# Optimization experiments

Hardware: AMD Instinct MI355X
Metric: run time of the kernel (lower is better)

The kernel has to match this reference:

```python
import jax, jax.numpy as jnp
import numpy as np

NUM_EMB = 10_000_000
EMB_DIM = 3
B = 16384
HIST = 50
K = 128


def setup_inputs() -> dict:
    key = jax.random.key(0)
    k1, k2, k3, k4, k5, k6, k7, k8, k9 = jax.random.split(key, 9)
    eb_input = jax.random.randint(k1, (B * HIST,), 0, NUM_EMB, dtype=jnp.int64)
    eb_offset = (jnp.arange(B, dtype=jnp.int64) * HIST)  # bag starts
    mlp_input = jax.random.normal(k2, (B, K), dtype=jnp.float32)
    # learned params
    emb_weight = jax.random.normal(k3, (NUM_EMB, EMB_DIM), dtype=jnp.float32)
    w0 = jax.random.normal(k4, (12, K), dtype=jnp.float32) * (1.0 / np.sqrt(K))
    b0 = jax.random.normal(k5, (12,), dtype=jnp.float32) * 0.01
    w1 = jax.random.normal(k6, (6, 12), dtype=jnp.float32) * (1.0 / np.sqrt(12))
    b1 = jax.random.normal(k7, (6,), dtype=jnp.float32) * 0.01
    w2 = jax.random.normal(k8, (3, 6), dtype=jnp.float32) * (1.0 / np.sqrt(6))
    b2 = jax.random.normal(k9, (3,), dtype=jnp.float32) * 0.01
    return {"eb_input": eb_input, "eb_offset": eb_offset, "mlp_input": mlp_input,
            "emb_weight": emb_weight, "w0": w0, "b0": b0, "w1": w1, "b1": b1,
            "w2": w2, "b2": b2}


def _embedding_bag_mean(weight, indices, offsets, num_bags):
    # bag id for each index position (offsets are sorted bag starts, offsets[0]=0)
    n = indices.shape[0]
    seg = jnp.searchsorted(offsets, jnp.arange(n, dtype=offsets.dtype), side='right') - 1
    rows = weight[indices]                                   # [N, 3] gather
    sums = jax.ops.segment_sum(rows, seg, num_segments=num_bags)          # [B, 3]
    cnts = jax.ops.segment_sum(jnp.ones((n,), weight.dtype), seg, num_segments=num_bags)
    return sums / jnp.maximum(cnts, 1.0)[:, None]            # mean mode; empty bag -> 0


def reference(eb_input, eb_offset, mlp_input, emb_weight, w0, b0, w1, b1, w2, b2):
    # All 3 EmbeddingBags alias the SAME module (python list * 3), so one lookup suffices.
    eb_out = _embedding_bag_mean(emb_weight, eb_input, eb_offset, mlp_input.shape[0])
    h = mlp_input @ w0.T + b0
    h = h @ w1.T + b1
    mlp_out = h @ w2.T + b2                                   # [B, 3]
    return jnp.concatenate([eb_out, eb_out, eb_out, mlp_out], axis=1)  # [B, 12]
```

## Files before the change

kernel.cpp:

```cpp
#include <hip/hip_runtime.h>


#define KDIM 128

__global__ __launch_bounds__(KDIM) void collapse_weights_kernel(
    const float* __restrict__ w0, const float* __restrict__ b0,
    const float* __restrict__ w1, const float* __restrict__ b1,
    const float* __restrict__ w2, const float* __restrict__ b2,
    float* __restrict__ ws)
{
    __shared__ float t[6][KDIM];
    __shared__ float tb[6];

    const int k = threadIdx.x;
    for (int i = 0; i < 6; ++i) {
        float acc = 0.f;
        for (int j = 0; j < 12; ++j)
            acc += w1[i * 12 + j] * w0[j * KDIM + k];
        t[i][k] = acc;
    }
    if (k < 6) {
        float acc = 0.f;
        for (int j = 0; j < 12; ++j)
            acc += w1[k * 12 + j] * b0[j];
        tb[k] = acc + b1[k];
    }
    __syncthreads();

    for (int o = 0; o < 3; ++o) {
        float acc = 0.f;
        for (int i = 0; i < 6; ++i)
            acc += w2[o * 6 + i] * t[i][k];
        ws[o * KDIM + k] = acc;
    }
    if (k == 0) {
        for (int o = 0; o < 3; ++o) {
            float acc = 0.f;
            for (int i = 0; i < 6; ++i)
                acc += w2[o * 6 + i] * tb[i];
            ws[3 * KDIM + o] = acc + b2[o];
        }
    }
}

__global__ __launch_bounds__(256) void fused_embbag_mlp_kernel(
    const int* __restrict__ eb_input,
    const int* __restrict__ eb_offset,
    const float* __restrict__ mlp_input,
    const float* __restrict__ emb_weight,
    const float* __restrict__ ws,
    float* __restrict__ out,
    int n_indices, int num_bags)
{
    const int lane = threadIdx.x & 63;
    const int wave = threadIdx.x >> 6;
    const int bag  = blockIdx.x * (blockDim.x >> 6) + wave;
    if (bag >= num_bags) return;

    const int start = eb_offset[bag];
    const int end   = (bag + 1 < num_bags) ? eb_offset[bag + 1] : n_indices;

    float s0 = 0.f, s1 = 0.f, s2 = 0.f;
    for (int i = start + lane; i < end; i += 64) {
        const int idx = eb_input[i];
        const float* r = emb_weight + (long long)idx * 3;
        s0 += r[0];
        s1 += r[1];
        s2 += r[2];
    }

    const float* x = mlp_input + (long long)bag * KDIM;
    const float2 xv = *(const float2*)(x + 2 * lane);
    const int c = 2 * lane;
    float m0 = xv.x * ws[0 * KDIM + c] + xv.y * ws[0 * KDIM + c + 1];
    float m1 = xv.x * ws[1 * KDIM + c] + xv.y * ws[1 * KDIM + c + 1];
    float m2 = xv.x * ws[2 * KDIM + c] + xv.y * ws[2 * KDIM + c + 1];

    #pragma unroll
    for (int off = 32; off > 0; off >>= 1) {
        s0 += __shfl_xor(s0, off, 64);
        s1 += __shfl_xor(s1, off, 64);
        s2 += __shfl_xor(s2, off, 64);
        m0 += __shfl_xor(m0, off, 64);
        m1 += __shfl_xor(m1, off, 64);
        m2 += __shfl_xor(m2, off, 64);
    }

    const float cnt = (float)(end - start);
    const float inv = 1.0f / fmaxf(cnt, 1.0f);
    const float e0 = s0 * inv, e1 = s1 * inv, e2 = s2 * inv;
    const float o9  = m0 + ws[3 * KDIM + 0];
    const float o10 = m1 + ws[3 * KDIM + 1];
    const float o11 = m2 + ws[3 * KDIM + 2];

    if (lane < 12) {
        float v;
        if (lane < 9) {
            const int r3 = lane - (lane >= 3 ? (lane >= 6 ? 6 : 3) : 0);
            v = (r3 == 0) ? e0 : (r3 == 1 ? e1 : e2);
        } else {
            v = (lane == 9) ? o9 : (lane == 10 ? o10 : o11);
        }
        out[(long long)bag * 12 + lane] = v;
    }
}

extern "C" void kernel_launch(void* const* d_in, const int* in_sizes, int n_in,
                              void* d_out, int out_size, void* d_ws, size_t ws_size,
                              hipStream_t stream) {
    const int*   eb_input   = (const int*)d_in[0];
    const int*   eb_offset  = (const int*)d_in[1];
    const float* mlp_input  = (const float*)d_in[2];
    const float* emb_weight = (const float*)d_in[3];
    const float* w0 = (const float*)d_in[4];
    const float* b0 = (const float*)d_in[5];
    const float* w1 = (const float*)d_in[6];
    const float* b1 = (const float*)d_in[7];
    const float* w2 = (const float*)d_in[8];
    const float* b2 = (const float*)d_in[9];
    float* out = (float*)d_out;
    float* ws  = (float*)d_ws;

    const int n_indices = in_sizes[0];
    const int num_bags  = in_sizes[1];

    collapse_weights_kernel<<<1, KDIM, 0, stream>>>(w0, b0, w1, b1, w2, b2, ws);

    const int waves_per_block = 4;
    const int grid = (num_bags + waves_per_block - 1) / waves_per_block;
    fused_embbag_mlp_kernel<<<grid, 256, 0, stream>>>(
        eb_input, eb_offset, mlp_input, emb_weight, ws, out, n_indices, num_bags);
}
```

Measured before the change: 198.5 us.

## Remap lanes to per-column gather and halve shuffle reduction work

Each wave now assigns lanes by (row group, embedding column), so each lane gathers a single float per row across 16 row groups instead of three floats per row. The MLP dot product is likewise split so each lane computes 8 elements for one output column with float4 loads. The cross-lane reduction then only reduces two values over 4 shuffle steps instead of six values over 6 steps, and the output write uses a direct lane-to-column mapping. In exchange each lane runs more loop iterations over the bag, which can expose more serialized gather latency, and one lane in four sits idle.

Result: no change. 199.7 us (+0.6%).

```diff
diff --git a/kernel.cpp b/kernel.cpp
--- a/kernel.cpp
+++ b/kernel.cpp
@@ -57,51 +57,40 @@
     const int bag  = blockIdx.x * (blockDim.x >> 6) + wave;
     if (bag >= num_bags) return;
 
+    const int c = lane & 3;
+    const int q = lane >> 2;
+
     const int start = eb_offset[bag];
     const int end   = (bag + 1 < num_bags) ? eb_offset[bag + 1] : n_indices;
+    const int cnt   = end - start;
 
-    float s0 = 0.f, s1 = 0.f, s2 = 0.f;
-    for (int i = start + lane; i < end; i += 64) {
-        const int idx = eb_input[i];
-        const float* r = emb_weight + (long long)idx * 3;
-        s0 += r[0];
-        s1 += r[1];
-        s2 += r[2];
+    float s = 0.f;
+    float m = 0.f;
+
+    if (c < 3) {
+        for (int row = q; row < cnt; row += 16) {
+            const int idx = eb_input[start + row];
+            s += emb_weight[(long long)idx * 3 + c];
+        }
+        const float4* xp = (const float4*)(mlp_input + (long long)bag * KDIM + q * 8);
+        const float4* wp = (const float4*)(ws + c * KDIM + q * 8);
+        const float4 x0 = xp[0], x1 = xp[1];
+        const float4 wv0 = wp[0], wv1 = wp[1];
+        m = x0.x * wv0.x + x0.y * wv0.y + x0.z * wv0.z + x0.w * wv0.w
+          + x1.x * wv1.x + x1.y * wv1.y + x1.z * wv1.z + x1.w * wv1.w;
     }
 
-    const float* x = mlp_input + (long long)bag * KDIM;
-    const float2 xv = *(const float2*)(x + 2 * lane);
-    const int c = 2 * lane;
-    float m0 = xv.x * ws[0 * KDIM + c] + xv.y * ws[0 * KDIM + c + 1];
-    float m1 = xv.x * ws[1 * KDIM + c] + xv.y * ws[1 * KDIM + c + 1];
-    float m2 = xv.x * ws[2 * KDIM + c] + xv.y * ws[2 * KDIM + c + 1];
-
     #pragma unroll
-    for (int off = 32; off > 0; off >>= 1) {
-        s0 += __shfl_xor(s0, off, 64);
-        s1 += __shfl_xor(s1, off, 64);
-        s2 += __shfl_xor(s2, off, 64);
-        m0 += __shfl_xor(m0, off, 64);
-        m1 += __shfl_xor(m1, off, 64);
-        m2 += __shfl_xor(m2, off, 64);
+    for (int off = 4; off <= 32; off <<= 1) {
+        s += __shfl_xor(s, off, 64);
+        m += __shfl_xor(m, off, 64);
     }
 
-    const float cnt = (float)(end - start);
-    const float inv = 1.0f / fmaxf(cnt, 1.0f);
-    const float e0 = s0 * inv, e1 = s1 * inv, e2 = s2 * inv;
-    const float o9  = m0 + ws[3 * KDIM + 0];
-    const float o10 = m1 + ws[3 * KDIM + 1];
-    const float o11 = m2 + ws[3 * KDIM + 2];
-
-    if (lane < 12) {
-        float v;
-        if (lane < 9) {
-            const int r3 = lane - (lane >= 3 ? (lane >= 6 ? 6 : 3) : 0);
-            v = (r3 == 0) ? e0 : (r3 == 1 ? e1 : e2);
-        } else {
-            v = (lane == 9) ? o9 : (lane == 10 ? o10 : o11);
-        }
-        out[(long long)bag * 12 + lane] = v;
+    if (c < 3 && q < 4) {
+        const float inv = 1.0f / fmaxf((float)cnt, 1.0f);
+        const int col = q * 3 + c;
+        const float v = (q < 3) ? s * inv : (m + ws[3 * KDIM + c]);
+        out[(long long)bag * 12 + col] = v;
     }
 }
 
```
